# Optimization experiments

Hardware: AMD Instinct MI355X
Metric: run time of the kernel (lower is better)

Reference implementation:

```python
import jax, jax.numpy as jnp
import numpy as np

EPS = 1e-8

def setup_inputs() -> dict:
    key = jax.random.key(0)
    k1, k2 = jax.random.split(key)
    B, IN, OUT, G = 32768, 256, 256, 5
    x = jax.random.normal(k1, (B, IN), dtype=jnp.float32)
    grid = jnp.linspace(-1.0, 1.0, G).astype(jnp.float32)
    coef = jax.random.normal(k2, (OUT, IN, G), dtype=jnp.float32) * 0.1
    scale = jnp.ones((OUT, IN), dtype=jnp.float32)
    bias = jnp.zeros((OUT,), dtype=jnp.float32)
    return {"x": x, "grid": grid, "coef": coef, "scale": scale, "bias": bias}

def reference(x, grid, coef, scale, bias):
    # global min-max normalization to [-1, 1]
    xmin, xmax = x.min(), x.max()
    xn = 2.0 * (x - xmin) / (xmax - xmin + EPS) - 1.0
    # cubic bump B-spline-like basis: (batch, in, grid)
    dist = jnp.abs(xn[..., None] - grid)
    basis = jnp.where(dist < 1.0, 1.0 - dist ** 3, 0.0)
    basis = basis / (basis.sum(axis=-1, keepdims=True) + EPS)
    # fused contraction over (in, grid); equals ((basis*coef).sum(-1)*scale).sum(-1)
    w = coef * scale[..., None]          # (out, in, grid)
    out = jnp.einsum('big,oig->bo', basis, w) + bias
    return out
```

## Files before the change

kernel.cpp:

```cpp
#include <hip/hip_runtime.h>
#include <stdint.h>


#define B_SZ   32768
#define IN_SZ  256
#define OUT_SZ 256
#define EPSF   1e-8f

#define A_STRIDE 40
#define AB_BUF   (128 * A_STRIDE)

typedef __bf16 bf16x8 __attribute__((ext_vector_type(8)));
typedef unsigned short ushort8 __attribute__((ext_vector_type(8)));
typedef float floatx16 __attribute__((ext_vector_type(16)));

__device__ __forceinline__ unsigned short f2bf(float f) {
  unsigned u = __float_as_uint(f);
  u += 0x7FFFu + ((u >> 16) & 1u);
  return (unsigned short)(u >> 16);
}


__global__ void __launch_bounds__(256) prep_kernel(const float* __restrict__ coef,
                                                   const float* __restrict__ scale,
                                                   const float* __restrict__ x,
                                                   unsigned short* __restrict__ wf,
                                                   float* __restrict__ part, int n4) {
  const int t = threadIdx.x;
  if (blockIdx.x < 256) {
    int idx = blockIdx.x * 256 + t;
    int o = idx >> 8, i = idx & 255;
    float s = scale[idx];
    const float* c = coef + (size_t)idx * 5;
    ushort8 v;
    v[0] = f2bf(c[0] * s); v[1] = f2bf(c[1] * s); v[2] = f2bf(c[2] * s);
    v[3] = f2bf(c[3] * s); v[4] = f2bf(c[4] * s);
    v[5] = 0; v[6] = 0; v[7] = 0;
    int chunk = (((o >> 5) * 64 + (i >> 2)) * 2 + ((i >> 1) & 1)) * 64
                + (i & 1) * 32 + (o & 31);
    *(ushort8*)(wf + (size_t)chunk * 8) = v;
  } else {
    int mb = blockIdx.x - 256;
    const float4* x4 = (const float4*)x;
    float lmin = 1e30f, lmax = -1e30f;
    for (int i = mb * 256 + t; i < n4; i += 256 * 256) {
      float4 v = x4[i];
      lmin = fminf(lmin, fminf(fminf(v.x, v.y), fminf(v.z, v.w)));
      lmax = fmaxf(lmax, fmaxf(fmaxf(v.x, v.y), fmaxf(v.z, v.w)));
    }
    #pragma unroll
    for (int off = 32; off >= 1; off >>= 1) {
      lmin = fminf(lmin, __shfl_down(lmin, off, 64));
      lmax = fmaxf(lmax, __shfl_down(lmax, off, 64));
    }
    __shared__ float smn[4], smx[4];
    if ((t & 63) == 0) { smn[t >> 6] = lmin; smx[t >> 6] = lmax; }
    __syncthreads();
    if (t == 0) {
      float mn = fminf(fminf(smn[0], smn[1]), fminf(smn[2], smn[3]));
      float mx = fmaxf(fmaxf(smx[0], smx[1]), fmaxf(smx[2], smx[3]));
      part[2 * mb] = mn;
      part[2 * mb + 1] = mx;
    }
  }
}

__global__ void __launch_bounds__(256, 2) kan_gemm(
    const float* __restrict__ x,
    const unsigned short* __restrict__ wf,
    const float* __restrict__ bias,
    const float* __restrict__ part,
    float* __restrict__ out)
{
  __shared__ __align__(16) unsigned short Ab[2 * AB_BUF];
  __shared__ float2 red[4];

  const int t = threadIdx.x;
  const int lane = t & 63;
  const int wv = t >> 6;
  const int wm = wv & 1, wn = wv >> 1;
  const int l31 = lane & 31, lh = lane >> 5;
  const int bRow = blockIdx.x * 128;
  const int bCol = blockIdx.y * 128;

  const int ogB = blockIdx.y * 4 + wn * 2;
  const unsigned short* wfl = wf + (size_t)lane * 8;
  auto loadB = [&](int kt, bf16x8 (*dst)[2]) {
    #pragma unroll
    for (int ks = 0; ks < 2; ++ks)
      #pragma unroll
      for (int ni = 0; ni < 2; ++ni)
        dst[ks][ni] = *(const bf16x8*)(wfl +
            (size_t)((((ogB + ni) * 64 + kt) * 2 + ks)) * 512);
  };

  const int arow = t >> 1;
  const int sl2 = (t & 1) * 2;
  const float* xrow = x + (size_t)(bRow + arow) * IN_SZ;
  unsigned short* awp = Ab + arow * A_STRIDE + sl2 * 8;

  bf16x8 bReg[2][2][2];
  loadB(0, bReg[0]);
  loadB(1, bReg[1]);
  float2 xv[2];
  xv[0] = *(const float2*)(xrow + 0 * 4 + sl2);
  xv[1] = *(const float2*)(xrow + 1 * 4 + sl2);

  float2 p = ((const float2*)part)[t];
  float mn = p.x, mx = p.y;
  #pragma unroll
  for (int off = 32; off >= 1; off >>= 1) {
    mn = fminf(mn, __shfl_down(mn, off, 64));
    mx = fmaxf(mx, __shfl_down(mx, off, 64));
  }
  if ((lane) == 0) red[wv] = make_float2(mn, mx);
  __syncthreads();
  mn = fminf(fminf(red[0].x, red[1].x), fminf(red[2].x, red[3].x));
  mx = fmaxf(fmaxf(red[0].y, red[1].y), fmaxf(red[2].y, red[3].y));
  const float scA = 2.0f / (mx - mn + EPSF);
  const float scB = -mn * scA - 1.0f;

  auto basis = [&](float2 xp, int buf) {
    #pragma unroll
    for (int j = 0; j < 2; ++j) {
      float xn = fmaf(j ? xp.y : xp.x, scA, scB);
      float d0 = xn + 1.0f, d1 = xn + 0.5f, d3 = xn - 0.5f, d4 = xn - 1.0f;
      float b0 = fmaxf(fmaf(d0 * d0, -fabsf(d0), 1.0f), 0.0f);
      float b1 = fmaxf(fmaf(d1 * d1, -fabsf(d1), 1.0f), 0.0f);
      float b2 = fmaxf(fmaf(xn * xn, -fabsf(xn), 1.0f), 0.0f);
      float b3 = fmaxf(fmaf(d3 * d3, -fabsf(d3), 1.0f), 0.0f);
      float b4 = fmaxf(fmaf(d4 * d4, -fabsf(d4), 1.0f), 0.0f);
      float sum = ((b0 + b1) + (b2 + b3)) + (b4 + EPSF);
      float inv = __builtin_amdgcn_rcpf(sum);
      bf16x8 av = {};
      av[0] = (__bf16)(b0 * inv); av[1] = (__bf16)(b1 * inv);
      av[2] = (__bf16)(b2 * inv); av[3] = (__bf16)(b3 * inv);
      av[4] = (__bf16)(b4 * inv);
      *(bf16x8*)(awp + buf * AB_BUF + j * 8) = av;
    }
  };

  basis(xv[0], 0);

  floatx16 acc[2][2] = {};

  for (int base = 0; base < 64; base += 2) {
    #pragma unroll
    for (int u = 0; u < 2; ++u) {
      const int kt = base + u;
      const int cur = u, nxt = u ^ 1;

      __syncthreads();

      bf16x8 af[2][2];
      #pragma unroll
      for (int ks = 0; ks < 2; ++ks)
        #pragma unroll
        for (int mi = 0; mi < 2; ++mi)
          af[ks][mi] = *(const bf16x8*)(Ab + cur * AB_BUF +
              (wm * 64 + mi * 32 + l31) * A_STRIDE + (ks * 2 + lh) * 8);

      if (kt < 63) basis(xv[nxt], nxt);

      #pragma unroll
      for (int ks = 0; ks < 2; ++ks)
        #pragma unroll
        for (int mi = 0; mi < 2; ++mi)
          #pragma unroll
          for (int ni = 0; ni < 2; ++ni)
            acc[mi][ni] = __builtin_amdgcn_mfma_f32_32x32x16_bf16(
                af[ks][mi], bReg[cur][ks][ni], acc[mi][ni], 0, 0, 0);

      if (kt < 62) {
        loadB(kt + 2, bReg[cur]);
        xv[cur] = *(const float2*)(xrow + (kt + 2) * 4 + sl2);
      }
    }
  }

  #pragma unroll
  for (int ni = 0; ni < 2; ++ni) {
    int o = bCol + wn * 64 + ni * 32 + l31;
    float bs = bias[o];
    #pragma unroll
    for (int mi = 0; mi < 2; ++mi) {
      int rb = bRow + wm * 64 + mi * 32 + 4 * lh;
      #pragma unroll
      for (int reg = 0; reg < 16; ++reg) {
        int row = rb + (reg & 3) + 8 * (reg >> 2);
        out[(size_t)row * OUT_SZ + o] = acc[mi][ni][reg] + bs;
      }
    }
  }
}

extern "C" void kernel_launch(void* const* d_in, const int* in_sizes, int n_in,
                              void* d_out, int out_size, void* d_ws, size_t ws_size,
                              hipStream_t stream) {
  const float* x     = (const float*)d_in[0];
  const float* coef  = (const float*)d_in[2];
  const float* scale = (const float*)d_in[3];
  const float* bias  = (const float*)d_in[4];
  float* out = (float*)d_out;

  size_t need = 4096 + (size_t)OUT_SZ * IN_SZ * 8 * 2;
  if (ws_size < need) return;

  float* part = (float*)d_ws;
  unsigned short* wf = (unsigned short*)((char*)d_ws + 4096);

  prep_kernel<<<512, 256, 0, stream>>>(coef, scale, x, wf, part,
                                       (B_SZ * IN_SZ) / 4);
  dim3 g(B_SZ / 128, OUT_SZ / 128);
  kan_gemm<<<g, 256, 0, stream>>>(x, wf, bias, part, out);
}
```

Before: 142.4 us.

## Compute basis fragments in registers per wave, drop LDS staging and barriers

```diff
diff --git a/kernel.cpp b/kernel.cpp
--- a/kernel.cpp
+++ b/kernel.cpp
@@ -7,12 +7,10 @@
 #define OUT_SZ 256
 #define EPSF   1e-8f
 
-#define A_STRIDE 40
-#define AB_BUF   (128 * A_STRIDE)
-
 typedef __bf16 bf16x8 __attribute__((ext_vector_type(8)));
 typedef unsigned short ushort8 __attribute__((ext_vector_type(8)));
 typedef float floatx16 __attribute__((ext_vector_type(16)));
+typedef float float2v __attribute__((ext_vector_type(2)));
 
 __device__ __forceinline__ unsigned short f2bf(float f) {
   unsigned u = __float_as_uint(f);
@@ -57,10 +55,8 @@
     if ((t & 63) == 0) { smn[t >> 6] = lmin; smx[t >> 6] = lmax; }
     __syncthreads();
     if (t == 0) {
-      float mn = fminf(fminf(smn[0], smn[1]), fminf(smn[2], smn[3]));
-      float mx = fmaxf(fmaxf(smx[0], smx[1]), fmaxf(smx[2], smx[3]));
-      part[2 * mb] = mn;
-      part[2 * mb + 1] = mx;
+      part[2 * mb]     = fminf(fminf(smn[0], smn[1]), fminf(smn[2], smn[3]));
+      part[2 * mb + 1] = fmaxf(fmaxf(smx[0], smx[1]), fmaxf(smx[2], smx[3]));
     }
   }
 }
@@ -72,39 +68,36 @@
     const float* __restrict__ part,
     float* __restrict__ out)
 {
-  __shared__ __align__(16) unsigned short Ab[2 * AB_BUF];
   __shared__ float2 red[4];
 
   const int t = threadIdx.x;
   const int lane = t & 63;
-  const int wv = t >> 6;
-  const int wm = wv & 1, wn = wv >> 1;
+  const int wm = t >> 6;
   const int l31 = lane & 31, lh = lane >> 5;
   const int bRow = blockIdx.x * 128;
   const int bCol = blockIdx.y * 128;
-
-  const int ogB = blockIdx.y * 4 + wn * 2;
-  const unsigned short* wfl = wf + (size_t)lane * 8;
-  auto loadB = [&](int kt, bf16x8 (*dst)[2]) {
+  const int row = bRow + wm * 32 + l31;
+
+  const unsigned short* bp[4];
+  #pragma unroll
+  for (int ni = 0; ni < 4; ++ni)
+    bp[ni] = wf + (size_t)(blockIdx.y * 4 + ni) * 65536 + (size_t)lane * 8;
+  const float* xp = x + (size_t)row * IN_SZ;
+
+  bf16x8 bReg[2][2][4];
+  float4 xq[2];
+  #pragma unroll
+  for (int u = 0; u < 2; ++u) {
+    xq[u] = *(const float4*)(xp + u * 4);
     #pragma unroll
     for (int ks = 0; ks < 2; ++ks)
       #pragma unroll
-      for (int ni = 0; ni < 2; ++ni)
-        dst[ks][ni] = *(const bf16x8*)(wfl +
-            (size_t)((((ogB + ni) * 64 + kt) * 2 + ks)) * 512);
-  };
-
-  const int arow = t >> 1;
-  const int sl2 = (t & 1) * 2;
-  const float* xrow = x + (size_t)(bRow + arow) * IN_SZ;
-  unsigned short* awp = Ab + arow * A_STRIDE + sl2 * 8;
-
-  bf16x8 bReg[2][2][2];
-  loadB(0, bReg[0]);
-  loadB(1, bReg[1]);
-  float2 xv[2];
-  xv[0] = *(const float2*)(xrow + 0 * 4 + sl2);
-  xv[1] = *(const float2*)(xrow + 1 * 4 + sl2);
+      for (int ni = 0; ni < 4; ++ni)
+        bReg[u][ks][ni] = *(const bf16x8*)(bp[ni] + u * 1024 + ks * 512);
+  }
+  xp += 8;
+  #pragma unroll
+  for (int ni = 0; ni < 4; ++ni) bp[ni] += 2048;
 
   float2 p = ((const float2*)part)[t];
   float mn = p.x, mx = p.y;
@@ -113,83 +106,77 @@
     mn = fminf(mn, __shfl_down(mn, off, 64));
     mx = fmaxf(mx, __shfl_down(mx, off, 64));
   }
-  if ((lane) == 0) red[wv] = make_float2(mn, mx);
+  if (lane == 0) red[wm] = make_float2(mn, mx);
   __syncthreads();
   mn = fminf(fminf(red[0].x, red[1].x), fminf(red[2].x, red[3].x));
   mx = fmaxf(fmaxf(red[0].y, red[1].y), fmaxf(red[2].y, red[3].y));
   const float scA = 2.0f / (mx - mn + EPSF);
   const float scB = -mn * scA - 1.0f;
 
-  auto basis = [&](float2 xp, int buf) {
-    #pragma unroll
-    for (int j = 0; j < 2; ++j) {
-      float xn = fmaf(j ? xp.y : xp.x, scA, scB);
-      float d0 = xn + 1.0f, d1 = xn + 0.5f, d3 = xn - 0.5f, d4 = xn - 1.0f;
-      float b0 = fmaxf(fmaf(d0 * d0, -fabsf(d0), 1.0f), 0.0f);
-      float b1 = fmaxf(fmaf(d1 * d1, -fabsf(d1), 1.0f), 0.0f);
-      float b2 = fmaxf(fmaf(xn * xn, -fabsf(xn), 1.0f), 0.0f);
-      float b3 = fmaxf(fmaf(d3 * d3, -fabsf(d3), 1.0f), 0.0f);
-      float b4 = fmaxf(fmaf(d4 * d4, -fabsf(d4), 1.0f), 0.0f);
-      float sum = ((b0 + b1) + (b2 + b3)) + (b4 + EPSF);
-      float inv = __builtin_amdgcn_rcpf(sum);
-      bf16x8 av = {};
-      av[0] = (__bf16)(b0 * inv); av[1] = (__bf16)(b1 * inv);
-      av[2] = (__bf16)(b2 * inv); av[3] = (__bf16)(b3 * inv);
-      av[4] = (__bf16)(b4 * inv);
-      *(bf16x8*)(awp + buf * AB_BUF + j * 8) = av;
-    }
+  auto basisfrag = [&](float xval) -> bf16x8 {
+    float xn = fmaf(xval, scA, scB);
+    float2v xx = {xn, xn};
+    float2v dA = xx + (float2v){1.0f, 0.5f};
+    float2v dB = xx - (float2v){0.5f, 1.0f};
+    float2v aA = __builtin_elementwise_max(dA, -dA);
+    float2v aB = __builtin_elementwise_max(dB, -dB);
+    float2v one2 = {1.0f, 1.0f};
+    float2v z2 = {0.0f, 0.0f};
+    float2v bA = __builtin_elementwise_max(one2 - dA * dA * aA, z2);
+    float2v bB = __builtin_elementwise_max(one2 - dB * dB * aB, z2);
+    float b2 = fmaxf(fmaf(xn * xn, -fabsf(xn), 1.0f), 0.0f);
+    float sum = (bA.x + bA.y) + (bB.x + bB.y) + (b2 + EPSF);
+    float inv = __builtin_amdgcn_rcpf(sum);
+    float2v sA = bA * inv;
+    float2v sB = bB * inv;
+    bf16x8 av = {};
+    av[0] = (__bf16)sA.x; av[1] = (__bf16)sA.y; av[2] = (__bf16)(b2 * inv);
+    av[3] = (__bf16)sB.x; av[4] = (__bf16)sB.y;
+    return av;
   };
 
-  basis(xv[0], 0);
-
-  floatx16 acc[2][2] = {};
+  floatx16 acc[4] = {};
 
   for (int base = 0; base < 64; base += 2) {
     #pragma unroll
     for (int u = 0; u < 2; ++u) {
       const int kt = base + u;
-      const int cur = u, nxt = u ^ 1;
-
-      __syncthreads();
-
-      bf16x8 af[2][2];
+
+      float xv0 = lh ? xq[u].y : xq[u].x;
+      float xv1 = lh ? xq[u].w : xq[u].z;
+      bf16x8 af0 = basisfrag(xv0);
+      bf16x8 af1 = basisfrag(xv1);
+
       #pragma unroll
-      for (int ks = 0; ks < 2; ++ks)
+      for (int ni = 0; ni < 4; ++ni)
+        acc[ni] = __builtin_amdgcn_mfma_f32_32x32x16_bf16(af0, bReg[u][0][ni], acc[ni], 0, 0, 0);
+      #pragma unroll
+      for (int ni = 0; ni < 4; ++ni)
+        acc[ni] = __builtin_amdgcn_mfma_f32_32x32x16_bf16(af1, bReg[u][1][ni], acc[ni], 0, 0, 0);
+
+      if (kt < 62) {
+        xq[u] = *(const float4*)(xp + u * 4);
         #pragma unroll
-        for (int mi = 0; mi < 2; ++mi)
-          af[ks][mi] = *(const bf16x8*)(Ab + cur * AB_BUF +
-              (wm * 64 + mi * 32 + l31) * A_STRIDE + (ks * 2 + lh) * 8);
-
-      if (kt < 63) basis(xv[nxt], nxt);
-
-      #pragma unroll
-      for (int ks = 0; ks < 2; ++ks)
-        #pragma unroll
-        for (int mi = 0; mi < 2; ++mi)
+        for (int ks = 0; ks < 2; ++ks)
           #pragma unroll
-          for (int ni = 0; ni < 2; ++ni)
-            acc[mi][ni] = __builtin_amdgcn_mfma_f32_32x32x16_bf16(
-                af[ks][mi], bReg[cur][ks][ni], acc[mi][ni], 0, 0, 0);
-
-      if (kt < 62) {
-        loadB(kt + 2, bReg[cur]);
-        xv[cur] = *(const float2*)(xrow + (kt + 2) * 4 + sl2);
+          for (int ni = 0; ni < 4; ++ni)
+            bReg[u][ks][ni] = *(const bf16x8*)(bp[ni] + u * 1024 + ks * 512);
       }
     }
-  }
-
-  #pragma unroll
-  for (int ni = 0; ni < 2; ++ni) {
-    int o = bCol + wn * 64 + ni * 32 + l31;
+    xp += 8;
+    #pragma unroll
+    for (int ni = 0; ni < 4; ++ni) bp[ni] += 2048;
+  }
+
+  #pragma unroll
+  for (int ni = 0; ni < 4; ++ni) {
+    int o = bCol + ni * 32 + l31;
     float bs = bias[o];
-    #pragma unroll
-    for (int mi = 0; mi < 2; ++mi) {
-      int rb = bRow + wm * 64 + mi * 32 + 4 * lh;
-      #pragma unroll
-      for (int reg = 0; reg < 16; ++reg) {
-        int row = rb + (reg & 3) + 8 * (reg >> 2);
-        out[(size_t)row * OUT_SZ + o] = acc[mi][ni][reg] + bs;
-      }
+    int rb = bRow + wm * 32 + 4 * lh;
+    #pragma unroll
+    for (int reg = 0; reg < 16; ++reg) {
+      int r = rb + (reg & 3) + 8 * (reg >> 2);
+      out[(size_t)r * OUT_SZ + o] = acc[ni][reg] + bs;
     }
   }
 }
```

Result: no change. 144.4 us (+1.4%).
